# Performance work log

Hardware: AMD Instinct MI355X
Metric: run time of the kernel (lower is better)

## Reference

```python
import jax, jax.numpy as jnp
import numpy as np

BSZ, SL, K, D_IN, D_OUT = 2, 1024, 24, 512, 512
K_U, K_Y = 3, 2
USE_HANKEL_L = False


def get_top_eigh(l, k, use_hankel_L):
    i = np.arange(1, l + 1, dtype=np.float64)
    s = i[:, None] + i[None, :]
    if use_hankel_L:
        Z = ((-1.0) ** (s - 2.0) + 1.0) * 8.0 / ((s + 3.0) * (s - 1.0) * (s + 1.0))
    else:
        Z = 2.0 / (s ** 3 - s)
    sigma, phi = np.linalg.eigh(Z)  # ascending
    return jnp.asarray(sigma[-k:], jnp.float32), jnp.asarray(phi[:, -k:], jnp.float32)


def shift(x, k):
    # causal shift along time axis 1, zero-padded at the front
    if k == 0:
        return x
    return jnp.pad(x, ((0, 0), (k, 0), (0, 0)))[:, : x.shape[1]]


def fft_causal_conv(filters, u):
    # filters: (l, k); u: (b, l, d) -> (b, l, k, d) causal convolution per filter
    l = u.shape[1]
    n = 2 * l
    F = jnp.fft.rfft(filters, n=n, axis=0)  # (n//2+1, k)
    U = jnp.fft.rfft(u, n=n, axis=1)        # (b, n//2+1, d)
    Y = jnp.fft.irfft(U[:, :, None, :] * F[None, :, :, None], n=n, axis=1)
    return Y[:, :l].astype(u.dtype)


def compute_ar_u(M_u, u):
    # ar_u[b,t,o] = sum_{i<k_u} M_u[i] @ u_{t-i}
    U = jnp.stack([shift(u, i) for i in range(M_u.shape[0])])  # (k_u, b, l, d_in)
    return jnp.einsum('koi,kbli->blo', M_u, U)


def compute_spectral(u, sigma, phi, M_phi_plus, M_phi_minus, m_y):
    l = u.shape[1]
    phi_s = phi * sigma ** 0.25  # eigenvalue-scaled spectral filters (l, k)
    U_plus = fft_causal_conv(phi_s, u)  # (b, l, k, d_in)
    spec = jnp.einsum('blki,koi->blo', U_plus, M_phi_plus)
    if not USE_HANKEL_L:
        # negative-featurization branch: filters modulated by (-1)^i
        alt = ((-1.0) ** jnp.arange(l)).astype(u.dtype)
        U_minus = fft_causal_conv(phi_s * alt[:, None], u)
        spec = spec + jnp.einsum('blki,koi->blo', U_minus, M_phi_minus)
    if m_y is not None:
        spec = shift(spec, m_y.shape[0])  # spectral features enter at lag k_y (paper: t-2)
    return spec


def compute_ar_y(m_y, y):
    # true short linear recurrence on outputs:
    # yhat_t = y_t + sum_{i=1}^{k_y} m_y[i-1] @ yhat_{t-i}; returns the correction term
    k_y, d_out = m_y.shape[0], m_y.shape[1]
    b = y.shape[0]

    def step(carry, y_t):  # carry: (k_y, b, d_out) = [yhat_{t-1}, ..., yhat_{t-k_y}]
        ar_t = jnp.einsum('koj,kbj->bo', m_y, carry)
        yhat_t = y_t + ar_t
        carry = jnp.concatenate([yhat_t[None], carry[:-1]], axis=0)
        return carry, ar_t

    y_tl = jnp.swapaxes(y, 0, 1)  # (l, b, d_out)
    _, ar = jax.lax.scan(step, jnp.zeros((k_y, b, d_out), y.dtype), y_tl)
    return jnp.swapaxes(ar, 0, 1)


def setup_inputs() -> dict:
    key = jax.random.key(0)
    k0, k1, k2, k3, k4 = jax.random.split(key, 5)
    inputs = jax.random.normal(k0, (BSZ, SL, D_IN), jnp.float32)
    M_u = jax.random.normal(k1, (K_U, D_OUT, D_IN), jnp.float32) * 0.02
    M_phi_plus = jax.random.normal(k2, (K, D_OUT, D_IN), jnp.float32) * 0.02
    M_phi_minus = jax.random.normal(k3, (K, D_OUT, D_IN), jnp.float32) * 0.02
    m_y = jax.random.normal(k4, (K_Y, D_OUT, D_OUT), jnp.float32) * 0.02
    sigma, phi = get_top_eigh(SL, K, USE_HANKEL_L)
    return {'inputs': inputs, 'M_u': M_u, 'M_phi_plus': M_phi_plus,
            'M_phi_minus': M_phi_minus, 'm_y': m_y, 'sigma': sigma, 'phi': phi}


def reference(inputs, M_u, M_phi_plus, M_phi_minus, m_y, sigma, phi):
    ar_u = compute_ar_u(M_u, inputs)
    spectral = compute_spectral(inputs, sigma, phi, M_phi_plus, M_phi_minus, m_y)
    y_t = ar_u + spectral
    y_t = y_t + compute_ar_y(m_y, y_t)  # learnable_m_y=True branch
    return y_t  # dropout p=0.0 (identity)
```

## Files before the change

kernel.cpp:

```cpp
#include <hip/hip_runtime.h>
#include <hip/hip_bf16.h>


typedef unsigned short u16;
typedef __attribute__((ext_vector_type(8))) short  vshort8;
typedef __attribute__((ext_vector_type(4))) short  vshort4;
typedef __attribute__((ext_vector_type(4))) float  f32x4;
typedef __attribute__((ext_vector_type(4))) unsigned int vuint4;

__device__ __forceinline__ u16 f2b(float x) {
  __hip_bfloat16 h = __float2bfloat16(x);
  return __builtin_bit_cast(u16, h);
}
__device__ __forceinline__ float b2f(u16 x) {
  unsigned int u = ((unsigned int)x) << 16;
  return __builtin_bit_cast(float, u);
}

struct GB {
  const u16* A; const u16* B;
  float* Cf; u16* Cb;
  const float* zf; float* out;
  u16* A2T; u16* Au;
  int M, N;
};

template<int V>
__global__ __launch_bounds__(256) void g2(GB a) {
  const int tid = threadIdx.x;
  int bn = blockIdx.x, bm = blockIdx.y;
  const int bz = blockIdx.z;
  int cj = 0, cb = 0, cd = 0, slot = 0;
  int kbeg = 0, kend = 0;
  if (V == 0) { bm = blockIdx.x; bn = blockIdx.y; kend = 512; }
  if (V == 1) {
    int p = blockIdx.x;
    bm = (int)((sqrtf(8.f * (float)p + 1.f) - 1.f) * 0.5f);
    cj = p - (bm * (bm + 1)) / 2;
    bn = blockIdx.y;
    cb = bz & 1; cd = bm - cj;
    slot = bz * 8 + cj;
    kbeg = (bz >> 1) * 3072; kend = kbeg + 3072;
  }
  const int m0 = bm * 128, n0 = bn * 128;
  if (V == 2) {
    int jmax = (m0 >> 6) + 1;
    kbeg = bz * 2048;
    kend = kbeg + 2048;
    int tk = (jmax + 1) * 512;
    if (kend > tk) kend = tk;
    if (kend < kbeg) kend = kbeg;
  }
  if (V == 3 || V == 5 || V == 6 || V == 7) kend = 1024;

  __shared__ u16 lA[2][4096], lB[2][4096];
  f32x4 acc[4][4];
#pragma unroll
  for (int i = 0; i < 4; i++)
#pragma unroll
    for (int j = 0; j < 4; j++) acc[i][j] = f32x4{0.f, 0.f, 0.f, 0.f};

  const int lane = tid & 63, wv = tid >> 6, wr = wv >> 1, wc = wv & 1;
  const u16* Ap = a.A;
  if (V == 5) Ap = a.A + (size_t)bz * 524288;

  auto gaddrA = [&](int it, int k0) -> const u16* {
    int lrow = (it * 4 + wv) * 16 + (lane & 15);
    int kk = k0 + ((lane >> 4) << 3);
    if (V == 0) return Ap + (size_t)(m0 + lrow) * 512 + kk;
    if (V == 1) return Ap + (size_t)cd * 786432 + (size_t)lrow * 6144 + kk;
    if (V == 2) {
      int m = m0 + lrow, j = m >> 6, b = (m >> 5) & 1, c = m & 31;
      int tau = kk >> 9, p = kk & 511;
      if (tau > j) return nullptr;
      return Ap + (size_t)(b * 1024 + c * 32 + j - tau) * 512 + p;
    }
    if (V == 3) { int m = m0 + lrow; return (m < a.M) ? Ap + (size_t)m * 1024 + kk : nullptr; }
    if (V == 5) return Ap + (size_t)(m0 + lrow) * 1024 + kk;
    if (V == 6) return (lrow < 64) ? Ap + (size_t)lrow * 1024 + kk : nullptr;
    if (lrow < 32) {
      int b = lrow & 1, k2 = lrow >> 1;
      return Ap + (size_t)(b * 32 + 2 * k2) * 1024 + kk;
    }
    return nullptr;
  };
  auto gaddrB = [&](int it, int k0) -> const u16* {
    int lrow = (it * 4 + wv) * 16 + (lane & 15);
    int kk = k0 + ((lane >> 4) << 3);
    int n = n0 + lrow;
    if (V == 0) return a.B + (size_t)n * 512 + kk;
    if (V == 1) {
      int kh = kk >> 7, sp = kk & 127;
      return a.B + (size_t)(cb * 512 + n) * 49152 + kh * 1024 + cj * 128 + sp;
    }
    if (V == 2) {
      int tau = kk >> 9, p = kk & 511;
      return a.B + (size_t)tau * 524288 + (size_t)n * 1024 + p;
    }
    if (V == 3) {
      int jn = n >> 9, o = n & 511;
      return a.B + (size_t)(jn + 1) * 524288 + (size_t)o * 1024 + kk;
    }
    if (V == 5) return a.B + (size_t)n * 1024 + kk;
    return (n < 512)
        ? a.B + (size_t)32 * 524288 + (size_t)n * 1024 + kk
        : a.B + (size_t)31 * 524288 + (size_t)(n - 512) * 1024 + kk;
  };

  vuint4 ra[2] = {vuint4{0,0,0,0}, vuint4{0,0,0,0}};
  vuint4 rb[2] = {vuint4{0,0,0,0}, vuint4{0,0,0,0}};
  auto loadtile = [&](int k0) {
#pragma unroll
    for (int it = 0; it < 2; ++it) {
      const u16* pa = gaddrA(it, k0);
      ra[it] = pa ? *(const vuint4*)pa : vuint4{0u, 0u, 0u, 0u};
      rb[it] = *(const vuint4*)gaddrB(it, k0);
    }
  };
  auto writetile = [&](int c) {
#pragma unroll
    for (int it = 0; it < 2; ++it) {
      *(vuint4*)&lA[c][it * 2048 + tid * 8] = ra[it];
      *(vuint4*)&lB[c][it * 2048 + tid * 8] = rb[it];
    }
  };

  if (kbeg < kend) loadtile(kbeg);
  writetile(0);
  __syncthreads();
  int cur = 0;
  for (int k0 = kbeg; k0 < kend; k0 += 32) {
    bool hasnext = (k0 + 32 < kend);
    if (hasnext) loadtile(k0 + 32);
    vshort8 af[4], bf_[4];
#pragma unroll
    for (int s = 0; s < 4; s++) {
      af[s]  = *(const vshort8*)&lA[cur][(((wr * 4 + s) * 4 + (lane >> 4)) * 16 + (lane & 15)) * 8];
      bf_[s] = *(const vshort8*)&lB[cur][(((wc * 4 + s) * 4 + (lane >> 4)) * 16 + (lane & 15)) * 8];
    }
#pragma unroll
    for (int i = 0; i < 4; i++)
#pragma unroll
      for (int j = 0; j < 4; j++)
        acc[i][j] = __builtin_amdgcn_mfma_f32_16x16x32_bf16(af[i], bf_[j], acc[i][j], 0, 0, 0);
    if (hasnext) writetile(cur ^ 1);
    __syncthreads();
    cur ^= 1;
  }

#pragma unroll
  for (int i = 0; i < 4; i++) {
    int em = m0 + wr * 64 + i * 16 + ((lane >> 4) << 2);
#pragma unroll
    for (int j = 0; j < 4; j++) {
      int n = n0 + wc * 64 + j * 16 + (lane & 15);
      f32x4 v = acc[i][j];
      if (V == 0) {
        int b = em >> 10, s = em & 1023;
        if (n < 24576) {
          int kh = n >> 9, o = n & 511;
          vshort4 pk = { (short)f2b(v[0]), (short)f2b(v[1]), (short)f2b(v[2]), (short)f2b(v[3]) };
          *(vshort4*)(&a.A2T[(size_t)(b * 512 + o) * 49152 + (size_t)kh * 1024 + s]) = pk;
        } else {
          int jj = (n - 24576) >> 9, o = n & 511;
#pragma unroll
          for (int t = 0; t < 4; t++)
            a.Au[((size_t)(b * 3 + jj) * 1024 + (s + t)) * 512 + o] = f2b(v[t]);
        }
      } else if (V == 1) {
        u16* C = a.Cb + (size_t)slot * 524288;
#pragma unroll
        for (int t = 0; t < 4; t++) C[(size_t)(em + t) * 512 + n] = f2b(v[t]);
      } else if (V == 2) {
        float* C = a.Cf + (size_t)bz * 1048576;
#pragma unroll
        for (int t = 0; t < 4; t++) C[(size_t)(em + t) * 512 + n] = v[t];
      } else if (V == 3) {
        int jj = n >> 9, oo = n & 511;
#pragma unroll
        for (int t = 0; t < 4; t++) {
          int m = em + t;
          if (m < a.M) {
            int b = m >> 5, c = m & 31;
            float zv = a.zf[(size_t)(jj * 64 + b * 32 + c) * 512 + oo];
            a.out[(size_t)b * 524288 + (size_t)(c * 32 + jj) * 512 + oo] = v[t] + zv;
          }
        }
      } else if (V == 5) {
        u16* C = a.Cb + (size_t)bz * 524288;
#pragma unroll
        for (int t = 0; t < 4; t++) C[(size_t)(em + t) * 1024 + n] = f2b(v[t]);
      } else if (V == 6) {
        int jrow = (n < 512) ? 31 : 30, oo = n & 511;
#pragma unroll
        for (int t = 0; t < 4; t++) {
          int m = em + t;
          if (m < 62) {
            int b = m & 1, c = m >> 1;
            a.Cf[(size_t)m * 1024 + n] =
                v[t] + a.zf[(size_t)(jrow * 64 + b * 32 + (c + 1)) * 512 + oo];
          }
        }
      } else {
        int jrow = (n < 512) ? 31 : 30, oo = n & 511;
#pragma unroll
        for (int t = 0; t < 4; t++) {
          int m = em + t;
          if (m < 32) {
            int b = m & 1, k2 = m >> 1;
            float val = v[t] + a.zf[(size_t)(jrow * 64 + b * 32 + 2 * k2) * 512 + oo];
            a.Cb[(size_t)(b * 32 + 2 * k2 + 1) * 1024 + n] = f2b(val);
          }
        }
      }
    }
  }
}

__global__ void k_prep_X(const float* __restrict__ u, u16* __restrict__ X, int n) {
  int i = blockIdx.x * 256 + threadIdx.x;
  if (i < n) X[i] = f2b(u[i]);
}

__global__ void k_prep_phis(const float* __restrict__ phi, const float* __restrict__ sigma,
                            float* __restrict__ phis) {
  int i = blockIdx.x * 256 + threadIdx.x;
  if (i >= 1024 * 48) return;
  int tau = i / 48, kf = i % 48, k = (kf >= 24) ? kf - 24 : kf;
  float v = phi[tau * 24 + k] * powf(sigma[k], 0.25f);
  if (kf >= 24 && (tau & 1)) v = -v;
  phis[i] = v;
}

__global__ void k_prep_W1(const float* __restrict__ Mp, const float* __restrict__ Mm,
                          const float* __restrict__ Mu, u16* __restrict__ W1) {
  int i = blockIdx.x * 256 + threadIdx.x;
  if (i >= 13369344) return;
  float v;
  if (i < 6291456) v = Mp[i];
  else if (i < 12582912) v = Mm[i - 6291456];
  else v = Mu[i - 12582912];
  W1[i] = f2b(v);
}

__global__ void k_prep_Wtoep(const float* __restrict__ phis, u16* __restrict__ W) {
  int i = blockIdx.x * 256 + threadIdx.x;
  if (i >= 6291456) return;
  int kap = i % 6144, row = i / 6144;
  int tp = row & 127, d = row >> 7;
  int kh = kap >> 7, sp = kap & 127;
  int tau = d * 128 + tp - sp;
  W[i] = (tau >= 0 && tau < 1024) ? f2b(phis[tau * 48 + kh]) : (u16)0;
}

__global__ void k_initTop(const float* __restrict__ my, u16* __restrict__ Top) {
  int i = blockIdx.x * 256 + threadIdx.x;
  if (i >= 1048576) return;
  int mat = i >> 19, rem = i & 524287, o = rem >> 10, k = rem & 1023;
  u16 v;
  if (mat == 0) v = (k == o) ? (u16)0x3F80 : (u16)0;
  else v = (k < 512) ? f2b(my[o * 512 + k]) : f2b(my[262144 + o * 512 + (k - 512)]);
  Top[i] = v;
}

__global__ __launch_bounds__(256) void k_transT(const u16* __restrict__ Top,
                                                u16* __restrict__ STc, int c) {
  __shared__ u16 tile[64][72];
  int tx = blockIdx.x, ty = blockIdx.y;
  int tid = threadIdx.x;
  int r = tid >> 2, seg = tid & 3;
  int k = ty * 64 + r;
  const u16* src = (k < 512) ? Top + (size_t)c * 524288 + (size_t)k * 1024 + tx * 64
                             : Top + (size_t)(c - 1) * 524288 + (size_t)(k - 512) * 1024 + tx * 64;
  *(vuint4*)&tile[r][seg * 16]     = *(const vuint4*)(src + seg * 16);
  *(vuint4*)&tile[r][seg * 16 + 8] = *(const vuint4*)(src + seg * 16 + 8);
  __syncthreads();
  int n = tx * 64 + r;
  u16 tmp[16];
#pragma unroll
  for (int j = 0; j < 16; j++) tmp[j] = tile[seg * 16 + j][r];
  *(vuint4*)&STc[(size_t)n * 1024 + ty * 64 + seg * 16]     = *(vuint4*)&tmp[0];
  *(vuint4*)&STc[(size_t)n * 1024 + ty * 64 + seg * 16 + 8] = *(vuint4*)&tmp[8];
}

__device__ __forceinline__ void addp(float* acc, vuint4 v) {
  const unsigned int* vu = (const unsigned int*)&v;
#pragma unroll
  for (int e = 0; e < 4; ++e) {
    unsigned int pw = vu[e];
    acc[2 * e]     += __builtin_bit_cast(float, (pw & 0xffffu) << 16);
    acc[2 * e + 1] += __builtin_bit_cast(float, pw & 0xffff0000u);
  }
}

__global__ void k_combine(const u16* __restrict__ parts, const u16* __restrict__ Au,
                          u16* __restrict__ ybf) {
  int i = blockIdx.x * 256 + threadIdx.x;
  if (i >= 131072) return;
  int og = i & 63, t = (i >> 6) & 1023, b = i >> 16;
  float acc[8];
#pragma unroll
  for (int e = 0; e < 8; ++e) acc[e] = 0.f;
#pragma unroll
  for (int j = 0; j < 3; j++)
    if (t >= j)
      addp(acc, *(const vuint4*)(Au + ((size_t)(b * 3 + j) * 1024 + (t - j)) * 512 + og * 8));
  if (t >= 2) {
    int tp = t - 2, bmv = tp >> 7;
#pragma unroll
    for (int g = 0; g < 4; ++g) {
      if ((g & 1) != b) continue;
      const u16* base = parts + (size_t)(g * 8) * 524288 + (size_t)tp * 512 + og * 8;
      for (int j = 0; j <= bmv; ++j)
        addp(acc, *(const vuint4*)(base + (size_t)j * 524288));
    }
  }
  u16 o16[8];
#pragma unroll
  for (int e = 0; e < 8; ++e) o16[e] = f2b(acc[e]);
  *(vuint4*)(ybf + ((size_t)(b * 1024 + t)) * 512 + og * 8) = *(vuint4*)o16;
}

__global__ void k_zreduce(const float* __restrict__ zp, float* __restrict__ z) {
  int i = blockIdx.x * 256 + threadIdx.x;
  if (i >= 1048576) return;
  float s = 0.f;
#pragma unroll
  for (int j = 0; j < 8; j++) s += zp[(size_t)j * 1048576 + i];
  z[i] = s;
}

__global__ void k_wm(const float* __restrict__ zf, u16* __restrict__ Wm) {
  int i = blockIdx.x * 256 + threadIdx.x;
  if (i >= 65536) return;
  int row = i >> 10, n = i & 1023;
  int b = row & 1, c = row >> 1;
  int jrow = (n < 512) ? 31 : 30, oo = n & 511;
  Wm[i] = f2b(zf[(size_t)(jrow * 64 + b * 32 + c) * 512 + oo]);
}

__global__ __launch_bounds__(256) void k_bnd2(const u16* __restrict__ Top,
                                              const float* __restrict__ ubuf,
                                              float* __restrict__ bnd,
                                              u16* __restrict__ Abnd, int k) {
  __shared__ float st[2048];
  int tid = threadIdx.x;
  const float* s0 = bnd + (size_t)k * 2048;
  for (int j = tid; j < 2048; j += 256) st[j] = s0[j];
  __syncthreads();
  int q4 = blockIdx.x * 256 + tid;
  int q = q4 >> 2, quarter = q4 & 3;
  int b = q >> 10, kk = q & 1023;
  const u16* row = (kk < 512) ? Top + (size_t)64 * 524288 + (size_t)kk * 1024
                              : Top + (size_t)63 * 524288 + (size_t)(kk - 512) * 1024;
  const float* stb = st + b * 1024 + quarter * 256;
  const u16* rp = row + quarter * 256;
  float sum = 0.f;
  for (int t = 0; t < 32; ++t) {
    vuint4 v = *(const vuint4*)(rp + t * 8);
    const unsigned int* vu = (const unsigned int*)&v;
#pragma unroll
    for (int e = 0; e < 4; ++e) {
      unsigned int pw = vu[e];
      float lo = __builtin_bit_cast(float, (pw & 0xffffu) << 16);
      float hi = __builtin_bit_cast(float, pw & 0xffff0000u);
      sum += lo * stb[t * 8 + e * 2] + hi * stb[t * 8 + e * 2 + 1];
    }
  }
  sum += __shfl_xor(sum, 1);
  sum += __shfl_xor(sum, 2);
  if (quarter == 0) {
    float s = sum + ubuf[(size_t)(4 * k + b) * 1024 + kk];
    bnd[(size_t)(k + 1) * 2048 + b * 1024 + kk] = s;
    Abnd[(size_t)(b * 32 + 2 * k + 2) * 1024 + kk] = f2b(s);
  }
}

extern "C" void kernel_launch(void* const* d_in, const int* in_sizes, int n_in,
                              void* d_out, int out_size, void* d_ws, size_t ws_size,
                              hipStream_t stream) {
  const float* u     = (const float*)d_in[0];
  const float* Mu    = (const float*)d_in[1];
  const float* Mp    = (const float*)d_in[2];
  const float* Mm    = (const float*)d_in[3];
  const float* my    = (const float*)d_in[4];
  const float* sigma = (const float*)d_in[5];
  const float* phi   = (const float*)d_in[6];
  float* out = (float*)d_out;

  char* ws = (char*)d_ws;
  size_t off = 0;
  auto alc = [&](size_t b) { size_t p = off; off = (off + b + 255) & ~(size_t)255; return p; };
  u16*  X     = (u16*)(ws + alc(2097152));
  u16*  Wtoep = (u16*)(ws + alc(12582912));
  u16*  A2T   = (u16*)(ws + alc(100663296));
  u16*  Au    = (u16*)(ws + alc(6291456));
  u16*  W1    = (u16*)(ws + alc(26738688));
  char* ptail = ws + alc(40370176); (void)ptail;
  float* phis = (float*)(ws + alc(196608));
  float* bnd  = (float*)(ws + alc(131072));
  u16*  Abnd  = (u16*)(ws + alc(131072));
  u16*  Wm    = (u16*)(ws + alc(131072));
  float* ubuf = (float*)(ws + alc(262144));
  if (off > ws_size) return;
  u16*  partsBf = (u16*)W1;
  float* zparts = (float*)W1;
  u16*  ybf = A2T;
  float* zf = (float*)((char*)A2T + (4 << 20));
  u16*  Top = (u16*)((char*)A2T + (size_t)(8 << 20));
  u16*  STc = (u16*)((char*)A2T + (size_t)(76 << 20));

  k_prep_X<<<dim3(4096), 256, 0, stream>>>(u, X, 1048576);
  k_prep_phis<<<dim3(192), 256, 0, stream>>>(phi, sigma, phis);
  k_prep_W1<<<dim3(52224), 256, 0, stream>>>(Mp, Mm, Mu, W1);
  k_prep_Wtoep<<<dim3(24576), 256, 0, stream>>>(phis, Wtoep);

  {
    GB g{}; g.A = X; g.B = W1; g.A2T = A2T; g.Au = Au;
    g.M = 2048; g.N = 26112;
    g2<0><<<dim3(16, 204, 1), 256, 0, stream>>>(g);
  }
  {
    GB g{}; g.A = Wtoep; g.B = A2T; g.Cb = partsBf;
    g.M = 1024; g.N = 512;
    g2<1><<<dim3(36, 4, 4), 256, 0, stream>>>(g);
  }
  k_combine<<<dim3(512), 256, 0, stream>>>(partsBf, Au, ybf);

  k_initTop<<<dim3(4096), 256, 0, stream>>>(my, Top);
  {
    const int cs[5] = {1, 2, 4, 8, 16};
    for (int li = 0; li < 5; ++li) {
      int c = cs[li];
      k_transT<<<dim3(16, 16), 256, 0, stream>>>(Top, STc, c);
      GB s{}; s.A = Top + 524288; s.B = STc; s.Cb = Top + (size_t)(c + 1) * 524288;
      s.M = 512; s.N = 1024;
      g2<5><<<dim3(8, 4, c), 256, 0, stream>>>(s);
    }
    k_transT<<<dim3(16, 16), 256, 0, stream>>>(Top, STc, 32);
    GB s{}; s.A = Top + (size_t)31 * 524288; s.B = STc;
    s.Cb = Top + (size_t)63 * 524288; s.M = 512; s.N = 1024;
    g2<5><<<dim3(8, 4, 2), 256, 0, stream>>>(s);
  }

  {
    GB g{}; g.A = ybf; g.B = Top; g.Cf = zparts; g.M = 2048; g.N = 512;
    g2<2><<<dim3(4, 16, 8), 256, 0, stream>>>(g);
  }
  k_zreduce<<<dim3(4096), 256, 0, stream>>>(zparts, zf);

  k_wm<<<dim3(256), 256, 0, stream>>>(zf, Wm);
  {
    GB g{}; g.A = Wm; g.B = Top; g.Cf = ubuf; g.zf = zf;
    g.M = 64; g.N = 1024;
    g2<6><<<dim3(8, 1, 1), 256, 0, stream>>>(g);
  }
  hipMemsetAsync(bnd, 0, 8192, stream);
  hipMemsetAsync(Abnd, 0, 131072, stream);
  for (int k = 0; k < 15; ++k)
    k_bnd2<<<dim3(32), 256, 0, stream>>>(Top, ubuf, bnd, Abnd, k);
  {
    GB g{}; g.A = Abnd; g.B = Top; g.Cb = Abnd; g.zf = zf;
    g.M = 32; g.N = 1024;
    g2<7><<<dim3(8, 1, 1), 256, 0, stream>>>(g);
  }

  {
    GB g{}; g.A = Abnd; g.B = Top; g.zf = zf; g.out = out;
    g.M = 64; g.N = 16384;
    g2<3><<<dim3(128, 1, 1), 256, 0, stream>>>(g);
  }
}
```

Measured before the change: 769.1 us.

## Build Toeplitz filter tiles in LDS and remap GEMM grids for XCD locality

Removes the materialised 12 MB Toeplitz weight matrix and its prep kernel. Each V1 GEMM block now stages a band of transposed spectral filters in shared memory and assembles A tiles from it on the fly. The V0, V1 and V2 GEMM grids are also flattened to 1D, with block indices permuted by (f&7) so consecutive tiles land on the same XCD for L2 reuse. The cost is extra LDS usage and scalar LDS gathers in the V1 load path.

```diff
diff --git a/kernel.cpp b/kernel.cpp
--- a/kernel.cpp
+++ b/kernel.cpp
@@ -22,6 +22,7 @@
   float* Cf; u16* Cb;
   const float* zf; float* out;
   u16* A2T; u16* Au;
+  const float* phisT;
   int M, N;
 };
 
@@ -29,23 +30,42 @@
 __global__ __launch_bounds__(256) void g2(GB a) {
   const int tid = threadIdx.x;
   int bn = blockIdx.x, bm = blockIdx.y;
-  const int bz = blockIdx.z;
+  int zz = blockIdx.z;
   int cj = 0, cb = 0, cd = 0, slot = 0;
   int kbeg = 0, kend = 0;
-  if (V == 0) { bm = blockIdx.x; bn = blockIdx.y; kend = 512; }
+  if (V == 0) {
+    int f = blockIdx.x;
+    int o = (f & 7) * 408 + (f >> 3);
+    bm = o & 15; bn = o >> 4; kend = 512;
+  }
   if (V == 1) {
-    int p = blockIdx.x;
-    bm = (int)((sqrtf(8.f * (float)p + 1.f) - 1.f) * 0.5f);
-    cj = p - (bm * (bm + 1)) / 2;
-    bn = blockIdx.y;
-    cb = bz & 1; cd = bm - cj;
-    slot = bz * 8 + cj;
-    kbeg = (bz >> 1) * 3072; kend = kbeg + 3072;
+    int f = blockIdx.x;
+    int o = (f & 7) * 72 + (f >> 3);
+    const int off1 = 128, off2 = 240, off3 = 336, off4 = 416,
+              off5 = 480, off6 = 528, off7 = 560;
+    cj = 0;
+    if (o >= off1) cj = 1; if (o >= off2) cj = 2; if (o >= off3) cj = 3;
+    if (o >= off4) cj = 4; if (o >= off5) cj = 5; if (o >= off6) cj = 6;
+    if (o >= off7) cj = 7;
+    const int offs[8] = {0, off1, off2, off3, off4, off5, off6, off7};
+    int r = o - offs[cj];
+    int run = 8 - cj;
+    int combo = r / run;
+    bm = cj + (r - combo * run);
+    zz = combo >> 2; bn = combo & 3;
+    cb = zz & 1; cd = bm - cj;
+    slot = zz * 8 + cj;
+    kbeg = (zz >> 1) * 3072; kend = kbeg + 3072;
+  }
+  if (V == 2) {
+    int f = blockIdx.x;
+    int o = (f & 7) * 64 + (f >> 3);
+    bm = o & 15; bn = (o >> 4) & 3; zz = o >> 6;
   }
   const int m0 = bm * 128, n0 = bn * 128;
   if (V == 2) {
     int jmax = (m0 >> 6) + 1;
-    kbeg = bz * 2048;
+    kbeg = zz * 2048;
     kend = kbeg + 2048;
     int tk = (jmax + 1) * 512;
     if (kend > tk) kend = tk;
@@ -54,6 +74,7 @@
   if (V == 3 || V == 5 || V == 6 || V == 7) kend = 1024;
 
   __shared__ u16 lA[2][4096], lB[2][4096];
+  __shared__ u16 band[V == 1 ? 12288 : 8];
   f32x4 acc[4][4];
 #pragma unroll
   for (int i = 0; i < 4; i++)
@@ -62,13 +83,21 @@
 
   const int lane = tid & 63, wv = tid >> 6, wr = wv >> 1, wc = wv & 1;
   const u16* Ap = a.A;
-  if (V == 5) Ap = a.A + (size_t)bz * 524288;
+  if (V == 5) Ap = a.A + (size_t)zz * 524288;
+
+  if (V == 1) {
+    for (int i = tid; i < 12288; i += 256) {
+      int kh = i >> 8, row = i & 255;
+      int tau = cd * 128 + row - 128;
+      band[i] = (tau >= 0) ? f2b(a.phisT[kh * 1024 + tau]) : (u16)0;
+    }
+    __syncthreads();
+  }
 
   auto gaddrA = [&](int it, int k0) -> const u16* {
     int lrow = (it * 4 + wv) * 16 + (lane & 15);
     int kk = k0 + ((lane >> 4) << 3);
     if (V == 0) return Ap + (size_t)(m0 + lrow) * 512 + kk;
-    if (V == 1) return Ap + (size_t)cd * 786432 + (size_t)lrow * 6144 + kk;
     if (V == 2) {
       int m = m0 + lrow, j = m >> 6, b = (m >> 5) & 1, c = m & 31;
       int tau = kk >> 9, p = kk & 511;
@@ -112,8 +141,23 @@
   auto loadtile = [&](int k0) {
 #pragma unroll
     for (int it = 0; it < 2; ++it) {
-      const u16* pa = gaddrA(it, k0);
-      ra[it] = pa ? *(const vuint4*)pa : vuint4{0u, 0u, 0u, 0u};
+      if (V == 1) {
+        int lrow = (it * 4 + wv) * 16 + (lane & 15);
+        int kk = k0 + ((lane >> 4) << 3);
+        int kh = kk >> 7, s0 = kk & 127;
+        int tr0 = kh * 256 + (lrow - s0 + 128);
+        unsigned int w32[4];
+#pragma unroll
+        for (int e2 = 0; e2 < 4; ++e2) {
+          unsigned int lo = band[tr0 - 2 * e2];
+          unsigned int hi = band[tr0 - 2 * e2 - 1];
+          w32[e2] = lo | (hi << 16);
+        }
+        ra[it] = vuint4{w32[0], w32[1], w32[2], w32[3]};
+      } else {
+        const u16* pa = gaddrA(it, k0);
+        ra[it] = pa ? *(const vuint4*)pa : vuint4{0u, 0u, 0u, 0u};
+      }
       rb[it] = *(const vuint4*)gaddrB(it, k0);
     }
   };
@@ -172,7 +216,7 @@
 #pragma unroll
         for (int t = 0; t < 4; t++) C[(size_t)(em + t) * 512 + n] = f2b(v[t]);
       } else if (V == 2) {
-        float* C = a.Cf + (size_t)bz * 1048576;
+        float* C = a.Cf + (size_t)zz * 1048576;
 #pragma unroll
         for (int t = 0; t < 4; t++) C[(size_t)(em + t) * 512 + n] = v[t];
       } else if (V == 3) {
@@ -187,7 +231,7 @@
           }
         }
       } else if (V == 5) {
-        u16* C = a.Cb + (size_t)bz * 524288;
+        u16* C = a.Cb + (size_t)zz * 524288;
 #pragma unroll
         for (int t = 0; t < 4; t++) C[(size_t)(em + t) * 1024 + n] = f2b(v[t]);
       } else if (V == 6) {
@@ -223,13 +267,13 @@
 }
 
 __global__ void k_prep_phis(const float* __restrict__ phi, const float* __restrict__ sigma,
-                            float* __restrict__ phis) {
+                            float* __restrict__ phisT) {
   int i = blockIdx.x * 256 + threadIdx.x;
   if (i >= 1024 * 48) return;
   int tau = i / 48, kf = i % 48, k = (kf >= 24) ? kf - 24 : kf;
   float v = phi[tau * 24 + k] * powf(sigma[k], 0.25f);
   if (kf >= 24 && (tau & 1)) v = -v;
-  phis[i] = v;
+  phisT[kf * 1024 + tau] = v;
 }
 
 __global__ void k_prep_W1(const float* __restrict__ Mp, const float* __restrict__ Mm,
@@ -241,16 +285,6 @@
   else if (i < 12582912) v = Mm[i - 6291456];
   else v = Mu[i - 12582912];
   W1[i] = f2b(v);
-}
-
-__global__ void k_prep_Wtoep(const float* __restrict__ phis, u16* __restrict__ W) {
-  int i = blockIdx.x * 256 + threadIdx.x;
-  if (i >= 6291456) return;
-  int kap = i % 6144, row = i / 6144;
-  int tp = row & 127, d = row >> 7;
-  int kh = kap >> 7, sp = kap & 127;
-  int tau = d * 128 + tp - sp;
-  W[i] = (tau >= 0 && tau < 1024) ? f2b(phis[tau * 48 + kh]) : (u16)0;
 }
 
 __global__ void k_initTop(const float* __restrict__ my, u16* __restrict__ Top) {
@@ -392,12 +426,11 @@
   size_t off = 0;
   auto alc = [&](size_t b) { size_t p = off; off = (off + b + 255) & ~(size_t)255; return p; };
   u16*  X     = (u16*)(ws + alc(2097152));
-  u16*  Wtoep = (u16*)(ws + alc(12582912));
   u16*  A2T   = (u16*)(ws + alc(100663296));
   u16*  Au    = (u16*)(ws + alc(6291456));
   u16*  W1    = (u16*)(ws + alc(26738688));
   char* ptail = ws + alc(40370176); (void)ptail;
-  float* phis = (float*)(ws + alc(196608));
+  float* phisT = (float*)(ws + alc(196608));
   float* bnd  = (float*)(ws + alc(131072));
   u16*  Abnd  = (u16*)(ws + alc(131072));
   u16*  Wm    = (u16*)(ws + alc(131072));
@@ -411,19 +444,18 @@
   u16*  STc = (u16*)((char*)A2T + (size_t)(76 << 20));
 
   k_prep_X<<<dim3(4096), 256, 0, stream>>>(u, X, 1048576);
-  k_prep_phis<<<dim3(192), 256, 0, stream>>>(phi, sigma, phis);
+  k_prep_phis<<<dim3(192), 256, 0, stream>>>(phi, sigma, phisT);
   k_prep_W1<<<dim3(52224), 256, 0, stream>>>(Mp, Mm, Mu, W1);
-  k_prep_Wtoep<<<dim3(24576), 256, 0, stream>>>(phis, Wtoep);
 
   {
     GB g{}; g.A = X; g.B = W1; g.A2T = A2T; g.Au = Au;
     g.M = 2048; g.N = 26112;
-    g2<0><<<dim3(16, 204, 1), 256, 0, stream>>>(g);
-  }
-  {
-    GB g{}; g.A = Wtoep; g.B = A2T; g.Cb = partsBf;
+    g2<0><<<dim3(3264), 256, 0, stream>>>(g);
+  }
+  {
+    GB g{}; g.B = A2T; g.Cb = partsBf; g.phisT = phisT;
     g.M = 1024; g.N = 512;
-    g2<1><<<dim3(36, 4, 4), 256, 0, stream>>>(g);
+    g2<1><<<dim3(576), 256, 0, stream>>>(g);
   }
   k_combine<<<dim3(512), 256, 0, stream>>>(partsBf, Au, ybf);
 
@@ -445,7 +477,7 @@
 
   {
     GB g{}; g.A = ybf; g.B = Top; g.Cf = zparts; g.M = 2048; g.N = 512;
-    g2<2><<<dim3(4, 16, 8), 256, 0, stream>>>(g);
+    g2<2><<<dim3(512), 256, 0, stream>>>(g);
   }
   k_zreduce<<<dim3(4096), 256, 0, stream>>>(zparts, zf);
 
```

After: 766.8 us. No clear change (-0.3%).

## Stage GEMM tiles with global_load_lds and rebalance triangular grids with XCD swizzle

Applied to the files above, without the earlier changes.

Replaces the register-staged global→LDS copy in the shared GEMM template with direct global_load_lds (16-byte) transfers, and uses a zero-filled pad buffer instead of null pointers for masked rows. The V0/V1/V2 launches become 1D grids remapped with an 8-way XCD-style swizzle. V1 and V2 are reorganised to enumerate only the useful triangular blocks with finer K-splits, and the reduction kernels are adjusted to match. This aims to cut register traffic and wasted blocks on causal structure, at the risk of slower LDS-DMA ordering and load imbalance.

```diff
diff --git a/kernel.cpp b/kernel.cpp
--- a/kernel.cpp
+++ b/kernel.cpp
@@ -17,11 +17,18 @@
   return __builtin_bit_cast(float, u);
 }
 
+__device__ __forceinline__ void gll16(const u16* g, u16* l) {
+  __builtin_amdgcn_global_load_lds((__attribute__((address_space(1))) void*)g,
+                                   (__attribute__((address_space(3))) void*)l,
+                                   16, 0, 0);
+}
+
 struct GB {
   const u16* A; const u16* B;
   float* Cf; u16* Cb;
   const float* zf; float* out;
   u16* A2T; u16* Au;
+  const u16* zp;
   int M, N;
 };
 
@@ -29,28 +36,50 @@
 __global__ __launch_bounds__(256) void g2(GB a) {
   const int tid = threadIdx.x;
   int bn = blockIdx.x, bm = blockIdx.y;
-  const int bz = blockIdx.z;
+  int zz = blockIdx.z;
   int cj = 0, cb = 0, cd = 0, slot = 0;
   int kbeg = 0, kend = 0;
-  if (V == 0) { bm = blockIdx.x; bn = blockIdx.y; kend = 512; }
+  if (V == 0) {
+    int f = blockIdx.x;
+    int o = (f & 7) * 408 + (f >> 3);
+    bm = o & 15; bn = o >> 4; kend = 512;
+  }
   if (V == 1) {
-    int p = blockIdx.x;
-    bm = (int)((sqrtf(8.f * (float)p + 1.f) - 1.f) * 0.5f);
-    cj = p - (bm * (bm + 1)) / 2;
-    bn = blockIdx.y;
-    cb = bz & 1; cd = bm - cj;
-    slot = bz * 8 + cj;
-    kbeg = (bz >> 1) * 3072; kend = kbeg + 3072;
+    int f = blockIdx.x;
+    int o = (f & 7) * 144 + (f >> 3);
+    const int offs1[8] = {0, 256, 480, 672, 832, 960, 1056, 1120};
+    cj = 0;
+    if (o >= offs1[1]) cj = 1;
+    if (o >= offs1[2]) cj = 2;
+    if (o >= offs1[3]) cj = 3;
+    if (o >= offs1[4]) cj = 4;
+    if (o >= offs1[5]) cj = 5;
+    if (o >= offs1[6]) cj = 6;
+    if (o >= offs1[7]) cj = 7;
+    int r = o - offs1[cj];
+    int run = 8 - cj;
+    int combo = r / run;
+    bm = cj + (r - combo * run);
+    int zzc = combo >> 2; bn = combo & 3;
+    cb = zzc & 1; cd = bm - cj;
+    slot = zzc * 8 + cj;
+    kbeg = (zzc >> 1) * 1536; kend = kbeg + 1536;
+  }
+  if (V == 2) {
+    int f = blockIdx.x;
+    int o = (f & 7) * 68 + (f >> 3);
+    const int offs2[16] = {0, 64, 124, 180, 232, 280, 324, 364,
+                           400, 432, 460, 484, 504, 520, 532, 540};
+    int s = 0;
+#pragma unroll
+    for (int c = 1; c < 16; ++c)
+      if (o >= offs2[c]) s = c;
+    int r = o - offs2[s];
+    bm = s + (r >> 2); bn = r & 3;
+    zz = s;
+    kbeg = s * 1024; kend = kbeg + 1024;
   }
   const int m0 = bm * 128, n0 = bn * 128;
-  if (V == 2) {
-    int jmax = (m0 >> 6) + 1;
-    kbeg = bz * 2048;
-    kend = kbeg + 2048;
-    int tk = (jmax + 1) * 512;
-    if (kend > tk) kend = tk;
-    if (kend < kbeg) kend = kbeg;
-  }
   if (V == 3 || V == 5 || V == 6 || V == 7) kend = 1024;
 
   __shared__ u16 lA[2][4096], lB[2][4096];
@@ -62,7 +91,8 @@
 
   const int lane = tid & 63, wv = tid >> 6, wr = wv >> 1, wc = wv & 1;
   const u16* Ap = a.A;
-  if (V == 5) Ap = a.A + (size_t)bz * 524288;
+  if (V == 5) Ap = a.A + (size_t)zz * 524288;
+  const u16* zpl = a.zp + lane * 8;
 
   auto gaddrA = [&](int it, int k0) -> const u16* {
     int lrow = (it * 4 + wv) * 16 + (lane & 15);
@@ -72,17 +102,17 @@
     if (V == 2) {
       int m = m0 + lrow, j = m >> 6, b = (m >> 5) & 1, c = m & 31;
       int tau = kk >> 9, p = kk & 511;
-      if (tau > j) return nullptr;
+      if (tau > j) return zpl;
       return Ap + (size_t)(b * 1024 + c * 32 + j - tau) * 512 + p;
     }
-    if (V == 3) { int m = m0 + lrow; return (m < a.M) ? Ap + (size_t)m * 1024 + kk : nullptr; }
+    if (V == 3) { int m = m0 + lrow; return (m < a.M) ? Ap + (size_t)m * 1024 + kk : zpl; }
     if (V == 5) return Ap + (size_t)(m0 + lrow) * 1024 + kk;
-    if (V == 6) return (lrow < 64) ? Ap + (size_t)lrow * 1024 + kk : nullptr;
+    if (V == 6) return (lrow < 64) ? Ap + (size_t)lrow * 1024 + kk : zpl;
     if (lrow < 32) {
       int b = lrow & 1, k2 = lrow >> 1;
       return Ap + (size_t)(b * 32 + 2 * k2) * 1024 + kk;
     }
-    return nullptr;
+    return zpl;
   };
   auto gaddrB = [&](int it, int k0) -> const u16* {
     int lrow = (it * 4 + wv) * 16 + (lane & 15);
@@ -107,31 +137,20 @@
         : a.B + (size_t)31 * 524288 + (size_t)(n - 512) * 1024 + kk;
   };
 
-  vuint4 ra[2] = {vuint4{0,0,0,0}, vuint4{0,0,0,0}};
-  vuint4 rb[2] = {vuint4{0,0,0,0}, vuint4{0,0,0,0}};
-  auto loadtile = [&](int k0) {
+  auto stage = [&](int c, int k0) {
 #pragma unroll
     for (int it = 0; it < 2; ++it) {
-      const u16* pa = gaddrA(it, k0);
-      ra[it] = pa ? *(const vuint4*)pa : vuint4{0u, 0u, 0u, 0u};
-      rb[it] = *(const vuint4*)gaddrB(it, k0);
+      int weff = wv + it * 4;
+      gll16(gaddrA(it, k0), &lA[c][weff * 512]);
+      gll16(gaddrB(it, k0), &lB[c][weff * 512]);
     }
   };
-  auto writetile = [&](int c) {
-#pragma unroll
-    for (int it = 0; it < 2; ++it) {
-      *(vuint4*)&lA[c][it * 2048 + tid * 8] = ra[it];
-      *(vuint4*)&lB[c][it * 2048 + tid * 8] = rb[it];
-    }
-  };
-
-  if (kbeg < kend) loadtile(kbeg);
-  writetile(0);
+
+  if (kbeg < kend) stage(0, kbeg);
   __syncthreads();
   int cur = 0;
   for (int k0 = kbeg; k0 < kend; k0 += 32) {
-    bool hasnext = (k0 + 32 < kend);
-    if (hasnext) loadtile(k0 + 32);
+    if (k0 + 32 < kend) stage(cur ^ 1, k0 + 32);
     vshort8 af[4], bf_[4];
 #pragma unroll
     for (int s = 0; s < 4; s++) {
@@ -143,7 +162,6 @@
 #pragma unroll
       for (int j = 0; j < 4; j++)
         acc[i][j] = __builtin_amdgcn_mfma_f32_16x16x32_bf16(af[i], bf_[j], acc[i][j], 0, 0, 0);
-    if (hasnext) writetile(cur ^ 1);
     __syncthreads();
     cur ^= 1;
   }
@@ -172,7 +190,7 @@
 #pragma unroll
         for (int t = 0; t < 4; t++) C[(size_t)(em + t) * 512 + n] = f2b(v[t]);
       } else if (V == 2) {
-        float* C = a.Cf + (size_t)bz * 1048576;
+        float* C = a.Cf + (size_t)zz * 1048576;
 #pragma unroll
         for (int t = 0; t < 4; t++) C[(size_t)(em + t) * 512 + n] = v[t];
       } else if (V == 3) {
@@ -187,7 +205,7 @@
           }
         }
       } else if (V == 5) {
-        u16* C = a.Cb + (size_t)bz * 524288;
+        u16* C = a.Cb + (size_t)zz * 524288;
 #pragma unroll
         for (int t = 0; t < 4; t++) C[(size_t)(em + t) * 1024 + n] = f2b(v[t]);
       } else if (V == 6) {
@@ -308,7 +326,7 @@
   if (t >= 2) {
     int tp = t - 2, bmv = tp >> 7;
 #pragma unroll
-    for (int g = 0; g < 4; ++g) {
+    for (int g = 0; g < 8; ++g) {
       if ((g & 1) != b) continue;
       const u16* base = parts + (size_t)(g * 8) * 524288 + (size_t)tp * 512 + og * 8;
       for (int j = 0; j <= bmv; ++j)
@@ -324,9 +342,9 @@
 __global__ void k_zreduce(const float* __restrict__ zp, float* __restrict__ z) {
   int i = blockIdx.x * 256 + threadIdx.x;
   if (i >= 1048576) return;
+  int nsum = (i >> 16) + 1;
   float s = 0.f;
-#pragma unroll
-  for (int j = 0; j < 8; j++) s += zp[(size_t)j * 1048576 + i];
+  for (int j = 0; j < nsum; ++j) s += zp[(size_t)j * 1048576 + i];
   z[i] = s;
 }
 
@@ -402,6 +420,7 @@
   u16*  Abnd  = (u16*)(ws + alc(131072));
   u16*  Wm    = (u16*)(ws + alc(131072));
   float* ubuf = (float*)(ws + alc(262144));
+  u16*  zpad  = (u16*)(ws + alc(32768));
   if (off > ws_size) return;
   u16*  partsBf = (u16*)W1;
   float* zparts = (float*)W1;
@@ -410,20 +429,22 @@
   u16*  Top = (u16*)((char*)A2T + (size_t)(8 << 20));
   u16*  STc = (u16*)((char*)A2T + (size_t)(76 << 20));
 
+  hipMemsetAsync(zpad, 0, 32768, stream);
+
   k_prep_X<<<dim3(4096), 256, 0, stream>>>(u, X, 1048576);
   k_prep_phis<<<dim3(192), 256, 0, stream>>>(phi, sigma, phis);
   k_prep_W1<<<dim3(52224), 256, 0, stream>>>(Mp, Mm, Mu, W1);
   k_prep_Wtoep<<<dim3(24576), 256, 0, stream>>>(phis, Wtoep);
 
   {
-    GB g{}; g.A = X; g.B = W1; g.A2T = A2T; g.Au = Au;
+    GB g{}; g.A = X; g.B = W1; g.A2T = A2T; g.Au = Au; g.zp = zpad;
     g.M = 2048; g.N = 26112;
-    g2<0><<<dim3(16, 204, 1), 256, 0, stream>>>(g);
-  }
-  {
-    GB g{}; g.A = Wtoep; g.B = A2T; g.Cb = partsBf;
+    g2<0><<<dim3(3264), 256, 0, stream>>>(g);
+  }
+  {
+    GB g{}; g.A = Wtoep; g.B = A2T; g.Cb = partsBf; g.zp = zpad;
     g.M = 1024; g.N = 512;
-    g2<1><<<dim3(36, 4, 4), 256, 0, stream>>>(g);
+    g2<1><<<dim3(1152), 256, 0, stream>>>(g);
   }
   k_combine<<<dim3(512), 256, 0, stream>>>(partsBf, Au, ybf);
 
@@ -434,24 +455,25 @@
       int c = cs[li];
       k_transT<<<dim3(16, 16), 256, 0, stream>>>(Top, STc, c);
       GB s{}; s.A = Top + 524288; s.B = STc; s.Cb = Top + (size_t)(c + 1) * 524288;
-      s.M = 512; s.N = 1024;
+      s.zp = zpad; s.M = 512; s.N = 1024;
       g2<5><<<dim3(8, 4, c), 256, 0, stream>>>(s);
     }
     k_transT<<<dim3(16, 16), 256, 0, stream>>>(Top, STc, 32);
     GB s{}; s.A = Top + (size_t)31 * 524288; s.B = STc;
-    s.Cb = Top + (size_t)63 * 524288; s.M = 512; s.N = 1024;
+    s.Cb = Top + (size_t)63 * 524288; s.zp = zpad; s.M = 512; s.N = 1024;
     g2<5><<<dim3(8, 4, 2), 256, 0, stream>>>(s);
   }
 
   {
-    GB g{}; g.A = ybf; g.B = Top; g.Cf = zparts; g.M = 2048; g.N = 512;
-    g2<2><<<dim3(4, 16, 8), 256, 0, stream>>>(g);
+    GB g{}; g.A = ybf; g.B = Top; g.Cf = zparts; g.zp = zpad;
+    g.M = 2048; g.N = 512;
+    g2<2><<<dim3(544), 256, 0, stream>>>(g);
   }
   k_zreduce<<<dim3(4096), 256, 0, stream>>>(zparts, zf);
 
   k_wm<<<dim3(256), 256, 0, stream>>>(zf, Wm);
   {
-    GB g{}; g.A = Wm; g.B = Top; g.Cf = ubuf; g.zf = zf;
+    GB g{}; g.A = Wm; g.B = Top; g.Cf = ubuf; g.zf = zf; g.zp = zpad;
     g.M = 64; g.N = 1024;
     g2<6><<<dim3(8, 1, 1), 256, 0, stream>>>(g);
   }
@@ -460,13 +482,13 @@
   for (int k = 0; k < 15; ++k)
     k_bnd2<<<dim3(32), 256, 0, stream>>>(Top, ubuf, bnd, Abnd, k);
   {
-    GB g{}; g.A = Abnd; g.B = Top; g.Cb = Abnd; g.zf = zf;
+    GB g{}; g.A = Abnd; g.B = Top; g.Cb = Abnd; g.zf = zf; g.zp = zpad;
     g.M = 32; g.N = 1024;
     g2<7><<<dim3(8, 1, 1), 256, 0, stream>>>(g);
   }
 
   {
-    GB g{}; g.A = Abnd; g.B = Top; g.zf = zf; g.out = out;
+    GB g{}; g.A = Abnd; g.B = Top; g.zf = zf; g.out = out; g.zp = zpad;
     g.M = 64; g.N = 16384;
     g2<3><<<dim3(128, 1, 1), 256, 0, stream>>>(g);
   }
```

After: 756.9 us. No clear change (-1.6%).
